# Kernel tuning notes

Hardware: AMD Instinct MI355X
Metric: run time of the kernel (lower is better)

## Reference

```python
import jax, jax.numpy as jnp
import numpy as np

B, S, D, H = 1, 4096, 1024, 16
HD = D // H  # 64


def setup_inputs() -> dict:
    key = jax.random.key(0)
    k1, k2, k3, k4, k5 = jax.random.split(key, 5)
    hidden_states = jax.random.normal(k1, (B, S, D), dtype=jnp.float32)
    # rotary frequencies: freqs_cis[s, j] = exp(i * s * theta^(-2j/HD)), stored as (cos, sin)
    inv_freq = 1.0 / (10000.0 ** (jnp.arange(0, HD, 2, dtype=jnp.float32) / HD))  # [HD/2]
    angles = jnp.arange(S, dtype=jnp.float32)[:, None] * inv_freq[None, :]        # [S, HD/2]
    freqs_cis = jnp.stack([jnp.cos(angles), jnp.sin(angles)], axis=-1)            # [S, HD/2, 2]
    attention_mask = jnp.ones((B, S), dtype=jnp.float32)
    scale = 1.0 / np.sqrt(D)
    wq = jax.random.normal(k2, (D, D), dtype=jnp.float32) * scale
    wk = jax.random.normal(k3, (D, D), dtype=jnp.float32) * scale
    wv = jax.random.normal(k4, (D, D), dtype=jnp.float32) * scale
    wo = jax.random.normal(k5, (D, D), dtype=jnp.float32) * scale
    return {"hidden_states": hidden_states, "freqs_cis": freqs_cis,
            "attention_mask": attention_mask, "wq": wq, "wk": wk, "wv": wv, "wo": wo}


def _apply_rope(x, freqs_cis):
    # x: [B, S, H, HD]; freqs_cis: [S, HD/2, 2] (cos, sin)
    b, s, h, hd = x.shape
    xr = x.reshape(b, s, h, hd // 2, 2)
    a, bb = xr[..., 0], xr[..., 1]
    cos = freqs_cis[None, :s, None, :, 0]
    sin = freqs_cis[None, :s, None, :, 1]
    out_r = a * cos - bb * sin
    out_i = a * sin + bb * cos
    return jnp.stack([out_r, out_i], axis=-1).reshape(b, s, h, hd)


def reference(hidden_states, freqs_cis, attention_mask, wq, wk, wv, wo):
    b, s, d = hidden_states.shape
    scaling = HD ** -0.5
    q = (hidden_states @ wq).reshape(b, s, H, HD)
    k = (hidden_states @ wk).reshape(b, s, H, HD)
    v = (hidden_states @ wv).reshape(b, s, H, HD)
    q = _apply_rope(q, freqs_cis)
    k = _apply_rope(k, freqs_cis)
    # [B, H, S, S] scores, exactly as the torch module materializes them
    scores = jnp.einsum('bqhd,bkhd->bhqk', q, k) * scaling
    mask_add = (1.0 - attention_mask)[:, None, None, :] * -10000.0  # [B,1,1,S]
    scores = scores + mask_add
    attn = jax.nn.softmax(scores.astype(jnp.float32), axis=-1).astype(q.dtype)
    out = jnp.einsum('bhqk,bkhd->bqhd', attn, v).reshape(b, s, d)
    return out @ wo
```

## Files before the change

### kernel.cpp

```cpp
#include <hip/hip_runtime.h>
#include <stdint.h>

#define S_LEN 4096
#define DMODEL 1024
#define NH 16
#define HDIM 64
#define LOG2E 1.44269504088896340736f

typedef __attribute__((ext_vector_type(8))) __bf16 bf16x8;
typedef __attribute__((ext_vector_type(4))) __bf16 bf16x4;
typedef __attribute__((ext_vector_type(2))) __bf16 bf16x2;
typedef __attribute__((ext_vector_type(4))) float f32x4;
typedef __attribute__((ext_vector_type(16))) float f32x16;
typedef __attribute__((ext_vector_type(4))) unsigned int uint32x4;

__global__ __launch_bounds__(256) void convert_f32_bf16(const float* __restrict__ src,
                                                        __bf16* __restrict__ dst) {
  int idx = blockIdx.x * 256 + threadIdx.x;
  f32x4 v = ((const f32x4*)src)[idx];
  bf16x4 o;
#pragma unroll
  for (int i = 0; i < 4; ++i) o[i] = (__bf16)v[i];
  ((bf16x4*)dst)[idx] = o;
}

template <typename T>
__global__ __launch_bounds__(256) void transpose_tiles(const T* __restrict__ src,
                                                       __bf16* __restrict__ dst,
                                                       int R, int C) {
  src += (size_t)blockIdx.z * R * C;
  dst += (size_t)blockIdx.z * R * C;
  __shared__ __bf16 tile[64][65];
  const int r0 = blockIdx.y * 64, c0 = blockIdx.x * 64;
  const int t = threadIdx.x;
  const int col = t & 63, rsub = t >> 6;
#pragma unroll
  for (int i = 0; i < 16; ++i) {
    int r = rsub + i * 4;
    tile[r][col] = (__bf16)src[(size_t)(r0 + r) * C + (c0 + col)];
  }
  __syncthreads();
#pragma unroll
  for (int i = 0; i < 16; ++i) {
    int r = rsub + i * 4;
    dst[(size_t)(c0 + r) * R + (r0 + col)] = tile[col][r];
  }
}

template <int EPI>
__global__ __launch_bounds__(256) void gemm_bt(const __bf16* __restrict__ A,
                                               const __bf16* __restrict__ BT,
                                               __bf16* __restrict__ Cq,
                                               __bf16* __restrict__ Ck,
                                               __bf16* __restrict__ Cv,
                                               float* __restrict__ Cout,
                                               int Kdim, int Ndim) {
  __shared__ __align__(16) __bf16 At[128][40];
  __shared__ __align__(16) __bf16 Bt[128][40];
  const int t = threadIdx.x;
  const int wave = t >> 6, lane = t & 63;
  const int wr = wave >> 1, wc = wave & 1;
  const int lrow = lane & 15, lk = lane >> 4;
  const int bm = blockIdx.x, bn = blockIdx.y;

  f32x4 acc[4][4];
#pragma unroll
  for (int i = 0; i < 4; ++i)
#pragma unroll
    for (int j = 0; j < 4; ++j) acc[i][j] = f32x4{0.f, 0.f, 0.f, 0.f};

  const int arow0 = bm * 128, brow0 = bn * 128;
  for (int k0 = 0; k0 < Kdim; k0 += 32) {
    __syncthreads();
#pragma unroll
    for (int u = 0; u < 2; ++u) {
      int idx = t + u * 256;
      int row = idx >> 2, col = (idx & 3) * 8;
      *(bf16x8*)&At[row][col] =
          *(const bf16x8*)&A[(size_t)(arow0 + row) * Kdim + (k0 + col)];
      *(bf16x8*)&Bt[row][col] =
          *(const bf16x8*)&BT[(size_t)(brow0 + row) * Kdim + (k0 + col)];
    }
    __syncthreads();
    bf16x8 af[4], bfr[4];
#pragma unroll
    for (int mi = 0; mi < 4; ++mi)
      af[mi] = *(const bf16x8*)&At[wr * 64 + mi * 16 + lrow][lk * 8];
#pragma unroll
    for (int ni = 0; ni < 4; ++ni)
      bfr[ni] = *(const bf16x8*)&Bt[wc * 64 + ni * 16 + lrow][lk * 8];
#pragma unroll
    for (int mi = 0; mi < 4; ++mi)
#pragma unroll
      for (int ni = 0; ni < 4; ++ni)
        acc[mi][ni] =
            __builtin_amdgcn_mfma_f32_16x16x32_bf16(af[mi], bfr[ni], acc[mi][ni], 0, 0, 0);
  }

  const int rb = bm * 128 + wr * 64 + lk * 4;
  const int cb = bn * 128 + wc * 64 + lrow;
#pragma unroll
  for (int mi = 0; mi < 4; ++mi)
#pragma unroll
    for (int ni = 0; ni < 4; ++ni) {
      int c = cb + ni * 16;
#pragma unroll
      for (int r = 0; r < 4; ++r) {
        int row = rb + mi * 16 + r;
        float v = acc[mi][ni][r];
        if (EPI == 0) {
          Cout[(size_t)row * Ndim + c] = v;
        } else {
          int type = c >> 10, d = c & 1023;
          int hh = d >> 6, hd = d & 63;
          __bf16* dp = (type == 0) ? Cq : (type == 1) ? Ck : Cv;
          dp[((size_t)hh * S_LEN + row) * HDIM + hd] = (__bf16)v;
        }
      }
    }
}

__global__ __launch_bounds__(256) void rope_kernel(__bf16* __restrict__ Q,
                                                   __bf16* __restrict__ Kb,
                                                   const float* __restrict__ freqs) {
  size_t idx = (size_t)blockIdx.x * 256 + threadIdx.x;
  int i = idx & 31;
  size_t rest = idx >> 5;
  int s = rest & 4095;
  int h = (int)(rest >> 12);
  float c = freqs[(s * 32 + i) * 2 + 0];
  float sn = freqs[(s * 32 + i) * 2 + 1];
  size_t base = ((size_t)h * S_LEN + s) * HDIM + 2 * i;
  float qa = (float)Q[base], qb = (float)Q[base + 1];
  Q[base] = (__bf16)(qa * c - qb * sn);
  Q[base + 1] = (__bf16)(qa * sn + qb * c);
  float ka = (float)Kb[base], kb2 = (float)Kb[base + 1];
  Kb[base] = (__bf16)(ka * c - kb2 * sn);
  Kb[base + 1] = (__bf16)(ka * sn + kb2 * c);
}

__global__ __launch_bounds__(512, 2) void attn_kernel(const __bf16* __restrict__ Q,
                                                      const __bf16* __restrict__ Kmat,
                                                      const __bf16* __restrict__ Vt,
                                                      const float* __restrict__ mask,
                                                      __bf16* __restrict__ AO) {
  __shared__ float maskL[S_LEN];
  __shared__ __align__(16) __bf16 Kl[2][64][64];
  __shared__ __align__(16) __bf16 Vl[2][64][64];

  const int t = threadIdx.x;
  const int id = blockIdx.x;
  const int swz = (id & 7) * 32 + (id >> 3);
  const int h = swz >> 4;
  const int qb = swz & 15;
  const int wave = t >> 6, lane = t & 63;
  const int lq = lane & 31, hi = lane >> 5;
  const int sw = lq & 7;

  const __bf16* Kh = Kmat + (size_t)h * S_LEN * HDIM;
  const __bf16* Vh = Vt + (size_t)h * HDIM * S_LEN;

  const int sr = t >> 3;
  const int sc = t & 7;
  const int scs = (sc ^ (sr & 7)) * 8;
  const __bf16* Kgb = Kh + (size_t)sr * HDIM + sc * 8;
  const __bf16* Vgb = Vh + (size_t)sr * S_LEN + sc * 8;

  uint32x4 kreg, vreg;
#pragma unroll
  for (int i = 0; i < 8; ++i) {
    int idx = t + i * 512;
    maskL[idx] = (1.0f - mask[idx]) * (-10000.0f * LOG2E);
  }
  kreg = *(const uint32x4*)(Kgb);
  vreg = *(const uint32x4*)(Vgb);
  *(uint32x4*)&Kl[0][sr][scs] = kreg;
  *(uint32x4*)&Vl[0][sr][scs] = vreg;

  const __bf16* Qh = Q + ((size_t)h * S_LEN + qb * 256 + wave * 32 + lq) * HDIM;
  bf16x8 qf[4];
#pragma unroll
  for (int ds = 0; ds < 4; ++ds) qf[ds] = *(const bf16x8*)(Qh + ds * 16 + hi * 8);

  __syncthreads();

  const float SCL = 0.125f * LOG2E;
  float m = -1e30f, l = 0.f;
  f32x16 o0, o1;
#pragma unroll
  for (int r = 0; r < 16; ++r) { o0[r] = 0.f; o1[r] = 0.f; }

  for (int it = 0; it < S_LEN / 64; ++it) {
    const int cur = it & 1;
    const int kb = it * 64;

    if (it < S_LEN / 64 - 1) {
      kreg = *(const uint32x4*)(Kgb + (size_t)(kb + 64) * HDIM);
      vreg = *(const uint32x4*)(Vgb + (kb + 64));
    }

    f32x16 p0, p1;
#pragma unroll
    for (int r = 0; r < 16; ++r) { p0[r] = 0.f; p1[r] = 0.f; }
#pragma unroll
    for (int ds = 0; ds < 4; ++ds) {
      int sg = ((ds << 1) | hi) ^ sw;
      bf16x8 kf0 = *(const bf16x8*)&Kl[cur][lq][sg * 8];
      p0 = __builtin_amdgcn_mfma_f32_32x32x16_bf16(kf0, qf[ds], p0, 0, 0, 0);
    }
#pragma unroll
    for (int ds = 0; ds < 4; ++ds) {
      int sg = ((ds << 1) | hi) ^ sw;
      bf16x8 kf1 = *(const bf16x8*)&Kl[cur][lq + 32][sg * 8];
      p1 = __builtin_amdgcn_mfma_f32_32x32x16_bf16(kf1, qf[ds], p1, 0, 0, 0);
    }

#pragma unroll
    for (int tq = 0; tq < 4; ++tq) {
      f32x4 ma0 = *(const f32x4*)&maskL[kb + tq * 8 + hi * 4];
      f32x4 ma1 = *(const f32x4*)&maskL[kb + 32 + tq * 8 + hi * 4];
#pragma unroll
      for (int c = 0; c < 4; ++c) {
        p0[tq * 4 + c] = fmaf(p0[tq * 4 + c], SCL, ma0[c]);
        p1[tq * 4 + c] = fmaf(p1[tq * 4 + c], SCL, ma1[c]);
      }
    }

    float mA, mB;
    {
      float u0 = fmaxf(fmaxf(p0[0], p0[1]), fmaxf(p0[2], p0[3]));
      float u1 = fmaxf(fmaxf(p0[4], p0[5]), fmaxf(p0[6], p0[7]));
      float u2 = fmaxf(fmaxf(p0[8], p0[9]), fmaxf(p0[10], p0[11]));
      float u3 = fmaxf(fmaxf(p0[12], p0[13]), fmaxf(p0[14], p0[15]));
      mA = fmaxf(fmaxf(u0, u1), fmaxf(u2, u3));
      float w0 = fmaxf(fmaxf(p1[0], p1[1]), fmaxf(p1[2], p1[3]));
      float w1 = fmaxf(fmaxf(p1[4], p1[5]), fmaxf(p1[6], p1[7]));
      float w2 = fmaxf(fmaxf(p1[8], p1[9]), fmaxf(p1[10], p1[11]));
      float w3 = fmaxf(fmaxf(p1[12], p1[13]), fmaxf(p1[14], p1[15]));
      mB = fmaxf(fmaxf(w0, w1), fmaxf(w2, w3));
    }
    float mx = fmaxf(mA, mB);
    mx = fmaxf(mx, __shfl_xor(mx, 32));

    if (!__all(mx <= m)) {
      float mn = fmaxf(m, mx);
      float al = exp2f(m - mn);
      m = mn;
      l *= al;
#pragma unroll
      for (int r = 0; r < 16; ++r) { o0[r] *= al; o1[r] *= al; }
    }

#pragma unroll
    for (int r = 0; r < 16; ++r) p0[r] = exp2f(p0[r] - m);
#pragma unroll
    for (int r = 0; r < 16; ++r) p1[r] = exp2f(p1[r] - m);
    {
      float a0 = (p0[0] + p0[1]) + (p0[2] + p0[3]);
      float a1 = (p0[4] + p0[5]) + (p0[6] + p0[7]);
      float a2 = (p0[8] + p0[9]) + (p0[10] + p0[11]);
      float a3 = (p0[12] + p0[13]) + (p0[14] + p0[15]);
      float b0 = (p1[0] + p1[1]) + (p1[2] + p1[3]);
      float b1 = (p1[4] + p1[5]) + (p1[6] + p1[7]);
      float b2 = (p1[8] + p1[9]) + (p1[10] + p1[11]);
      float b3 = (p1[12] + p1[13]) + (p1[14] + p1[15]);
      float ps = ((a0 + a1) + (a2 + a3)) + ((b0 + b1) + (b2 + b3));
      ps += __shfl_xor(ps, 32);
      l += ps;
    }

    unsigned int tt0[8], tt1[8];
#pragma unroll
    for (int tp = 0; tp < 8; ++tp) {
      bf16x2 w0, w1;
      w0[0] = (__bf16)p0[2 * tp]; w0[1] = (__bf16)p0[2 * tp + 1];
      w1[0] = (__bf16)p1[2 * tp]; w1[1] = (__bf16)p1[2 * tp + 1];
      tt0[tp] = __builtin_bit_cast(unsigned int, w0);
      tt1[tp] = __builtin_bit_cast(unsigned int, w1);
    }

#pragma unroll
    for (int ks = 0; ks < 4; ++ks) {
      unsigned int b0, b1, b2, b3;
      if (ks == 0)      { b0 = tt0[0]; b1 = tt0[1]; b2 = tt0[2]; b3 = tt0[3]; }
      else if (ks == 1) { b0 = tt0[4]; b1 = tt0[5]; b2 = tt0[6]; b3 = tt0[7]; }
      else if (ks == 2) { b0 = tt1[0]; b1 = tt1[1]; b2 = tt1[2]; b3 = tt1[3]; }
      else              { b0 = tt1[4]; b1 = tt1[5]; b2 = tt1[6]; b3 = tt1[7]; }
      unsigned int x0 = (unsigned int)__shfl_xor((int)b0, 32);
      unsigned int x1 = (unsigned int)__shfl_xor((int)b1, 32);
      unsigned int x2 = (unsigned int)__shfl_xor((int)b2, 32);
      unsigned int x3 = (unsigned int)__shfl_xor((int)b3, 32);
      uint32x4 pb;
      pb[0] = hi ? x2 : b0;
      pb[1] = hi ? x3 : b1;
      pb[2] = hi ? b2 : x0;
      pb[3] = hi ? b3 : x1;
      bf16x8 pbv = __builtin_bit_cast(bf16x8, pb);
      int sg = ((ks << 1) | hi) ^ sw;
      bf16x8 v0 = *(const bf16x8*)&Vl[cur][lq][sg * 8];
      bf16x8 v1 = *(const bf16x8*)&Vl[cur][lq + 32][sg * 8];
      o0 = __builtin_amdgcn_mfma_f32_32x32x16_bf16(v0, pbv, o0, 0, 0, 0);
      o1 = __builtin_amdgcn_mfma_f32_32x32x16_bf16(v1, pbv, o1, 0, 0, 0);
    }

    if (it < S_LEN / 64 - 1) {
      *(uint32x4*)&Kl[cur ^ 1][sr][scs] = kreg;
      *(uint32x4*)&Vl[cur ^ 1][sr][scs] = vreg;
      __syncthreads();
    }
  }

  float inv = 1.0f / fmaxf(l, 1e-30f);
  __bf16* aorow = AO + (size_t)(qb * 256 + wave * 32 + lq) * DMODEL + h * HDIM;
#pragma unroll
  for (int tq = 0; tq < 4; ++tq) {
    bf16x4 ov0, ov1;
#pragma unroll
    for (int c = 0; c < 4; ++c) {
      ov0[c] = (__bf16)(o0[tq * 4 + c] * inv);
      ov1[c] = (__bf16)(o1[tq * 4 + c] * inv);
    }
    *(bf16x4*)(aorow + tq * 8 + hi * 4) = ov0;
    *(bf16x4*)(aorow + 32 + tq * 8 + hi * 4) = ov1;
  }
}

extern "C" void kernel_launch(void* const* d_in, const int* in_sizes, int n_in,
                              void* d_out, int out_size, void* d_ws, size_t ws_size,
                              hipStream_t stream) {
  const float* X = (const float*)d_in[0];
  const float* freqs = (const float*)d_in[1];
  const float* mask = (const float*)d_in[2];
  const float* wq = (const float*)d_in[3];
  const float* wk = (const float*)d_in[4];
  const float* wv = (const float*)d_in[5];
  const float* wo = (const float*)d_in[6];
  float* out = (float*)d_out;

  __bf16* WTqkv = (__bf16*)d_ws;
  __bf16* WoT = WTqkv + 3072 * 1024;
  __bf16* Xb = WoT + 1024 * 1024;
  __bf16* Qb = Xb + (size_t)S_LEN * DMODEL;
  __bf16* Kb = Qb + (size_t)NH * S_LEN * HDIM;
  __bf16* Vb = Kb + (size_t)NH * S_LEN * HDIM;
  __bf16* Vtb = Vb + (size_t)NH * S_LEN * HDIM;
  __bf16* AO = Vb;

  convert_f32_bf16<<<dim3(S_LEN * DMODEL / 1024), 256, 0, stream>>>(X, Xb);

  transpose_tiles<float><<<dim3(16, 16, 1), 256, 0, stream>>>(wq, WTqkv, 1024, 1024);
  transpose_tiles<float><<<dim3(16, 16, 1), 256, 0, stream>>>(wk, WTqkv + 1024 * 1024, 1024, 1024);
  transpose_tiles<float><<<dim3(16, 16, 1), 256, 0, stream>>>(wv, WTqkv + 2 * 1024 * 1024, 1024, 1024);
  transpose_tiles<float><<<dim3(16, 16, 1), 256, 0, stream>>>(wo, WoT, 1024, 1024);

  gemm_bt<1><<<dim3(32, 24), 256, 0, stream>>>(Xb, WTqkv, Qb, Kb, Vb, nullptr, 1024, 3072);

  rope_kernel<<<dim3((NH * S_LEN * 32) / 256), 256, 0, stream>>>(Qb, Kb, freqs);

  transpose_tiles<__bf16><<<dim3(1, 64, NH), 256, 0, stream>>>(Vb, Vtb, S_LEN, HDIM);

  attn_kernel<<<dim3(256), 512, 0, stream>>>(Qb, Kb, Vtb, mask, AO);

  gemm_bt<0><<<dim3(32, 8), 256, 0, stream>>>(AO, WoT, nullptr, nullptr, nullptr, out, 1024, 1024);
}
```

Before: 230.0 us.

## Use 128-row attention blocks with 4 waves, setprio around MFMAs, halve shuffles

Attention blocks shrink from 512 to 256 threads, each covering 128 query rows, and the grid doubles to 512 blocks. Each thread now stages two 16-byte chunks of K and V per tile. The aim is better load balance across CUs and more independent blocks per CU. The change also raises wave priority around the MFMA sections and sends only the needed halves in the P-matrix lane exchange, cutting four shuffles to two. The trade-off is twice the K/V tile loading per query row and more mask setup per block.

```diff
diff --git a/kernel.cpp b/kernel.cpp
--- a/kernel.cpp
+++ b/kernel.cpp
@@ -139,7 +139,7 @@
   Kb[base + 1] = (__bf16)(ka * sn + kb2 * c);
 }
 
-__global__ __launch_bounds__(512, 2) void attn_kernel(const __bf16* __restrict__ Q,
+__global__ __launch_bounds__(256, 2) void attn_kernel(const __bf16* __restrict__ Q,
                                                       const __bf16* __restrict__ Kmat,
                                                       const __bf16* __restrict__ Vt,
                                                       const float* __restrict__ mask,
@@ -150,9 +150,9 @@
 
   const int t = threadIdx.x;
   const int id = blockIdx.x;
-  const int swz = (id & 7) * 32 + (id >> 3);
-  const int h = swz >> 4;
-  const int qb = swz & 15;
+  const int swz = (id & 7) * 64 + (id >> 3);
+  const int h = swz >> 5;
+  const int qb = swz & 31;
   const int wave = t >> 6, lane = t & 63;
   const int lq = lane & 31, hi = lane >> 5;
   const int sw = lq & 7;
@@ -160,24 +160,29 @@
   const __bf16* Kh = Kmat + (size_t)h * S_LEN * HDIM;
   const __bf16* Vh = Vt + (size_t)h * HDIM * S_LEN;
 
-  const int sr = t >> 3;
-  const int sc = t & 7;
-  const int scs = (sc ^ (sr & 7)) * 8;
-  const __bf16* Kgb = Kh + (size_t)sr * HDIM + sc * 8;
-  const __bf16* Vgb = Vh + (size_t)sr * S_LEN + sc * 8;
-
-  uint32x4 kreg, vreg;
-#pragma unroll
-  for (int i = 0; i < 8; ++i) {
-    int idx = t + i * 512;
+  const int sr = t >> 2;
+  const int sc0 = (t & 3) * 2;
+  const int scs0 = (sc0 ^ (sr & 7)) * 8;
+  const int scs1 = ((sc0 + 1) ^ (sr & 7)) * 8;
+  const __bf16* Kgb = Kh + (size_t)sr * HDIM + sc0 * 8;
+  const __bf16* Vgb = Vh + (size_t)sr * S_LEN + sc0 * 8;
+
+  uint32x4 kreg0, kreg1, vreg0, vreg1;
+#pragma unroll
+  for (int i = 0; i < 16; ++i) {
+    int idx = t + i * 256;
     maskL[idx] = (1.0f - mask[idx]) * (-10000.0f * LOG2E);
   }
-  kreg = *(const uint32x4*)(Kgb);
-  vreg = *(const uint32x4*)(Vgb);
-  *(uint32x4*)&Kl[0][sr][scs] = kreg;
-  *(uint32x4*)&Vl[0][sr][scs] = vreg;
-
-  const __bf16* Qh = Q + ((size_t)h * S_LEN + qb * 256 + wave * 32 + lq) * HDIM;
+  kreg0 = *(const uint32x4*)(Kgb);
+  kreg1 = *(const uint32x4*)(Kgb + 8);
+  vreg0 = *(const uint32x4*)(Vgb);
+  vreg1 = *(const uint32x4*)(Vgb + 8);
+  *(uint32x4*)&Kl[0][sr][scs0] = kreg0;
+  *(uint32x4*)&Kl[0][sr][scs1] = kreg1;
+  *(uint32x4*)&Vl[0][sr][scs0] = vreg0;
+  *(uint32x4*)&Vl[0][sr][scs1] = vreg1;
+
+  const __bf16* Qh = Q + ((size_t)h * S_LEN + qb * 128 + wave * 32 + lq) * HDIM;
   bf16x8 qf[4];
 #pragma unroll
   for (int ds = 0; ds < 4; ++ds) qf[ds] = *(const bf16x8*)(Qh + ds * 16 + hi * 8);
@@ -195,13 +200,16 @@
     const int kb = it * 64;
 
     if (it < S_LEN / 64 - 1) {
-      kreg = *(const uint32x4*)(Kgb + (size_t)(kb + 64) * HDIM);
-      vreg = *(const uint32x4*)(Vgb + (kb + 64));
+      kreg0 = *(const uint32x4*)(Kgb + (size_t)(kb + 64) * HDIM);
+      kreg1 = *(const uint32x4*)(Kgb + (size_t)(kb + 64) * HDIM + 8);
+      vreg0 = *(const uint32x4*)(Vgb + (kb + 64));
+      vreg1 = *(const uint32x4*)(Vgb + (kb + 64) + 8);
     }
 
     f32x16 p0, p1;
 #pragma unroll
     for (int r = 0; r < 16; ++r) { p0[r] = 0.f; p1[r] = 0.f; }
+    __builtin_amdgcn_s_setprio(1);
 #pragma unroll
     for (int ds = 0; ds < 4; ++ds) {
       int sg = ((ds << 1) | hi) ^ sw;
@@ -214,6 +222,7 @@
       bf16x8 kf1 = *(const bf16x8*)&Kl[cur][lq + 32][sg * 8];
       p1 = __builtin_amdgcn_mfma_f32_32x32x16_bf16(kf1, qf[ds], p1, 0, 0, 0);
     }
+    __builtin_amdgcn_s_setprio(0);
 
 #pragma unroll
     for (int tq = 0; tq < 4; ++tq) {
@@ -286,32 +295,36 @@
       else if (ks == 1) { b0 = tt0[4]; b1 = tt0[5]; b2 = tt0[6]; b3 = tt0[7]; }
       else if (ks == 2) { b0 = tt1[0]; b1 = tt1[1]; b2 = tt1[2]; b3 = tt1[3]; }
       else              { b0 = tt1[4]; b1 = tt1[5]; b2 = tt1[6]; b3 = tt1[7]; }
-      unsigned int x0 = (unsigned int)__shfl_xor((int)b0, 32);
-      unsigned int x1 = (unsigned int)__shfl_xor((int)b1, 32);
-      unsigned int x2 = (unsigned int)__shfl_xor((int)b2, 32);
-      unsigned int x3 = (unsigned int)__shfl_xor((int)b3, 32);
+      unsigned int send0 = hi ? b0 : b2;
+      unsigned int send1 = hi ? b1 : b3;
+      unsigned int r0 = (unsigned int)__shfl_xor((int)send0, 32);
+      unsigned int r1 = (unsigned int)__shfl_xor((int)send1, 32);
       uint32x4 pb;
-      pb[0] = hi ? x2 : b0;
-      pb[1] = hi ? x3 : b1;
-      pb[2] = hi ? b2 : x0;
-      pb[3] = hi ? b3 : x1;
+      pb[0] = hi ? r0 : b0;
+      pb[1] = hi ? r1 : b1;
+      pb[2] = hi ? b2 : r0;
+      pb[3] = hi ? b3 : r1;
       bf16x8 pbv = __builtin_bit_cast(bf16x8, pb);
       int sg = ((ks << 1) | hi) ^ sw;
       bf16x8 v0 = *(const bf16x8*)&Vl[cur][lq][sg * 8];
       bf16x8 v1 = *(const bf16x8*)&Vl[cur][lq + 32][sg * 8];
+      __builtin_amdgcn_s_setprio(1);
       o0 = __builtin_amdgcn_mfma_f32_32x32x16_bf16(v0, pbv, o0, 0, 0, 0);
       o1 = __builtin_amdgcn_mfma_f32_32x32x16_bf16(v1, pbv, o1, 0, 0, 0);
+      __builtin_amdgcn_s_setprio(0);
     }
 
     if (it < S_LEN / 64 - 1) {
-      *(uint32x4*)&Kl[cur ^ 1][sr][scs] = kreg;
-      *(uint32x4*)&Vl[cur ^ 1][sr][scs] = vreg;
+      *(uint32x4*)&Kl[cur ^ 1][sr][scs0] = kreg0;
+      *(uint32x4*)&Kl[cur ^ 1][sr][scs1] = kreg1;
+      *(uint32x4*)&Vl[cur ^ 1][sr][scs0] = vreg0;
+      *(uint32x4*)&Vl[cur ^ 1][sr][scs1] = vreg1;
       __syncthreads();
     }
   }
 
   float inv = 1.0f / fmaxf(l, 1e-30f);
-  __bf16* aorow = AO + (size_t)(qb * 256 + wave * 32 + lq) * DMODEL + h * HDIM;
+  __bf16* aorow = AO + (size_t)(qb * 128 + wave * 32 + lq) * DMODEL + h * HDIM;
 #pragma unroll
   for (int tq = 0; tq < 4; ++tq) {
     bf16x4 ov0, ov1;
@@ -359,7 +372,7 @@
 
   transpose_tiles<__bf16><<<dim3(1, 64, NH), 256, 0, stream>>>(Vb, Vtb, S_LEN, HDIM);
 
-  attn_kernel<<<dim3(256), 512, 0, stream>>>(Qb, Kb, Vtb, mask, AO);
+  attn_kernel<<<dim3(512), 256, 0, stream>>>(Qb, Kb, Vtb, mask, AO);
 
   gemm_bt<0><<<dim3(32, 8), 256, 0, stream>>>(AO, WoT, nullptr, nullptr, nullptr, out, 1024, 1024);
 }
```

New measurement: 230.2 us. No clear change (+0.1%).
